# Optimization experiments

Measured on AMD Instinct MI355X. Metric: run time of the kernel, lower is better.

## Reference

```python
import jax, jax.numpy as jnp
import numpy as np

HEADS = 7
DIM_HEAD = 64
SCALE = DIM_HEAD ** -0.5


def setup_inputs() -> dict:
    key = jax.random.key(0)
    ks = jax.random.split(key, 6)
    b, n, dim = 8, 1024, 448
    inner = HEADS * DIM_HEAD  # 448
    x = jax.random.normal(ks[0], (b, n, dim), dtype=jnp.float32)
    w_qv = jax.random.normal(ks[1], (dim, 2 * inner), dtype=jnp.float32) * 0.02
    ext_k = jax.random.normal(ks[2], (HEADS, n, DIM_HEAD), dtype=jnp.float32)
    ext_bias = jax.random.normal(ks[3], (HEADS, n, n), dtype=jnp.float32)
    w_out = jax.random.normal(ks[4], (inner, dim), dtype=jnp.float32) * 0.02
    b_out = jnp.zeros((dim,), dtype=jnp.float32)
    return {"x": x, "w_qv": w_qv, "ext_k": ext_k, "ext_bias": ext_bias,
            "w_out": w_out, "b_out": b_out}


def reference(x, w_qv, ext_k, ext_bias, w_out, b_out):
    b, n, dim = x.shape
    qv = x @ w_qv                                   # [b, n, 2*inner]
    q, v = jnp.split(qv, 2, axis=-1)
    # b n (h d) -> b h n d
    q = q.reshape(b, n, HEADS, DIM_HEAD).transpose(0, 2, 1, 3)
    v = v.reshape(b, n, HEADS, DIM_HEAD).transpose(0, 2, 1, 3)
    # scores vs external learned key, additive bias applied BEFORE scale
    dots = (jnp.einsum('bhnd,hmd->bhnm', q, ext_k) + ext_bias[None]) * SCALE
    attn = jax.nn.softmax(dots, axis=-1)
    out = jnp.einsum('bhnm,bhmd->bhnd', attn, v)
    out = out.transpose(0, 2, 1, 3).reshape(b, n, HEADS * DIM_HEAD)
    return out @ w_out + b_out  # dropout is identity in eval mode
```

## Files before the change

kernel.cpp:

```cpp
#include <hip/hip_runtime.h>
#include <hip/hip_bf16.h>
#include <hip/hip_fp16.h>

#define BATCH 8
#define NSEQ 1024
#define DIMM 448
#define NHEAD 7
#define HDIM 64
#define MROWS (BATCH*NSEQ)
#define KDIM 448
#define SCALE_F 0.125f
#define PSTR 66048

typedef short short8 __attribute__((ext_vector_type(8)));
typedef float floatx16 __attribute__((ext_vector_type(16)));

#define MFMA32(a,b,c) __builtin_amdgcn_mfma_f32_32x32x16_bf16(a,b,c,0,0,0)

__device__ __forceinline__ unsigned short f2bf(float f){
    __hip_bfloat16 h = __float2bfloat16(f);
    return *reinterpret_cast<unsigned short*>(&h);
}
__device__ __forceinline__ float bf2f(unsigned short u){
    __hip_bfloat16 h; *reinterpret_cast<unsigned short*>(&h) = u;
    return __bfloat162float(h);
}
__device__ __forceinline__ float h2f(unsigned short u){
    __half h; *reinterpret_cast<unsigned short*>(&h) = u;
    return __half2float(h);
}
__device__ __forceinline__ unsigned short f2h(float f){
    __half h = __float2half(f);
    return *reinterpret_cast<unsigned short*>(&h);
}

__global__ __launch_bounds__(256)
void prep_all(const float* __restrict__ x, const float* __restrict__ ek,
              const float* __restrict__ wqv, const float* __restrict__ wout,
              const float* __restrict__ eb,
              unsigned short* __restrict__ xh, unsigned short* __restrict__ ekh,
              unsigned short* __restrict__ wqvTh, unsigned short* __restrict__ woTh,
              unsigned short* __restrict__ woTl, unsigned short* __restrict__ bp)
{
    __shared__ float T[2][64][33];
    const int bx = blockIdx.x, tid = threadIdx.x;

    if (bx < 3584) {
        int i = bx*256 + tid;
        float4 v = ((const float4*)x)[i];
        ((ushort4*)xh)[i] = make_ushort4(f2bf(v.x), f2bf(v.y), f2bf(v.z), f2bf(v.w));
    } else if (bx < 4032) {
        int i = (bx-3584)*256 + tid;
        const int h  = i >> 14, mm = (i >> 9) & 31, c = (i >> 7) & 3;
        const int ln = (i >> 1) & 63, jh = i & 1;
        const float* src = ek + ((size_t)(h*NSEQ) + mm*32 + (ln & 31))*HDIM
                              + c*16 + (ln >> 5)*8 + jh*4;
        float4 v = *(const float4*)src;
        unsigned short* dst = ekh + (size_t)h*PSTR + (size_t)(i & 16383)*4;
        *(ushort4*)dst = make_ushort4(f2bf(v.x), f2bf(v.y), f2bf(v.z), f2bf(v.w));
    } else if (bx < 4228) {
        int lid = (bx-4032)*4 + (tid>>6);
        int kc = lid % 56, ng = lid / 56;
        int n = ng*64 + (tid&63);
        unsigned short h[8];
#pragma unroll
        for (int j = 0; j < 8; ++j) h[j] = f2bf(wqv[(size_t)(kc*8+j)*896 + n]);
        size_t o = (size_t)n*KDIM + kc*8;
        *(ushort4*)(wqvTh + o)     = make_ushort4(h[0],h[1],h[2],h[3]);
        *(ushort4*)(wqvTh + o + 4) = make_ushort4(h[4],h[5],h[6],h[7]);
    } else if (bx < 4340) {
        int lid = (bx-4228)*4 + (tid>>6);
        int kc = lid % 56, ng = lid / 56;
        int n = ng*64 + (tid&63);
        ushort4 h0={0,0,0,0}, h1={0,0,0,0}, l0={0,0,0,0}, l1={0,0,0,0};
        if (n < DIMM) {
            unsigned short h[8], l[8];
#pragma unroll
            for (int j = 0; j < 8; ++j) {
                float f = wout[(size_t)(kc*8+j)*DIMM + n];
                h[j] = f2bf(f); l[j] = f2bf(f - bf2f(h[j]));
            }
            h0 = make_ushort4(h[0],h[1],h[2],h[3]); h1 = make_ushort4(h[4],h[5],h[6],h[7]);
            l0 = make_ushort4(l[0],l[1],l[2],l[3]); l1 = make_ushort4(l[4],l[5],l[6],l[7]);
        }
        size_t o = (size_t)n*KDIM + kc*8;
        *(ushort4*)(woTh + o) = h0; *(ushort4*)(woTh + o + 4) = h1;
        *(ushort4*)(woTl + o) = l0; *(ushort4*)(woTl + o + 4) = l1;
    } else {
        const int sub = tid >> 7, st = tid & 127;
        const int lid = (bx-4340)*2 + sub;
        const int mt = lid & 31, qt = (lid>>5) & 15, h = lid >> 9;
#pragma unroll
        for (int it = 0; it < 4; ++it) {
            int idx = it*128 + st;
            int row = idx >> 3, c4 = (idx & 7)*4;
            float4 v = *(const float4*)(eb + ((size_t)(h*NSEQ + qt*64 + row))*NSEQ + mt*32 + c4);
            T[sub][row][c4+0]=v.x; T[sub][row][c4+1]=v.y;
            T[sub][row][c4+2]=v.z; T[sub][row][c4+3]=v.w;
        }
        __syncthreads();
        const int g2 = st >> 6, lane = st & 63;
        const int lq = lane & 31, quad = lane >> 5;
        const int q = g2*32 + lq;
        unsigned short* dst = bp + (size_t)(h*16 + qt)*PSTR
                            + (size_t)(mt*4 + g2*2)*512 + lane*8;
#pragma unroll
        for (int jj = 0; jj < 2; ++jj) {
            unsigned short o[8];
#pragma unroll
            for (int t = 0; t < 8; ++t) {
                int m = (t&3) + 8*(t>>2) + 16*jj + 4*quad;
                o[t] = f2h(T[sub][q][m] * SCALE_F);
            }
            *(ushort4*)(dst + jj*512)     = make_ushort4(o[0],o[1],o[2],o[3]);
            *(ushort4*)(dst + jj*512 + 4) = make_ushort4(o[4],o[5],o[6],o[7]);
        }
    }
}

__global__ __launch_bounds__(256, 2)
void gemm1_grp(const unsigned short* __restrict__ Ah, const unsigned short* __restrict__ Bh,
               unsigned short* __restrict__ qd, unsigned short* __restrict__ vTd)
{
    const int tid = threadIdx.x;
    const int w = tid >> 6, lane = tid & 63;
    const int lq = lane & 31, lh = lane >> 5;
    const int m0 = (blockIdx.x*4 + w) * 64;
    const int y  = blockIdx.y;
    const int n0 = y * 64;
    const unsigned short* aB = Ah + (size_t)(m0 + lq)*KDIM + lh*8;
    const unsigned short* bB = Bh + (size_t)(n0 + lq)*KDIM + lh*8;

    floatx16 acc[2][2] = {};
    short8 aR[2][2][2], bR[2][2][2];
#define LD1(kt, par) {                                                        \
    _Pragma("unroll") for (int fm = 0; fm < 2; ++fm)                          \
    _Pragma("unroll") for (int c = 0; c < 2; ++c) {                           \
        aR[par][fm][c] = *(const short8*)(aB + (size_t)fm*32*KDIM + (kt)*32 + c*16); \
        bR[par][fm][c] = *(const short8*)(bB + (size_t)fm*32*KDIM + (kt)*32 + c*16); } }

    LD1(0, 0)
#pragma unroll
    for (int kt = 0; kt < 14; ++kt) {
        const int par = kt & 1;
        if (kt < 13) LD1(kt+1, par^1)
#pragma unroll
        for (int c = 0; c < 2; ++c)
#pragma unroll
            for (int fm = 0; fm < 2; ++fm)
#pragma unroll
                for (int fn = 0; fn < 2; ++fn)
                    acc[fm][fn] = MFMA32(aR[par][fm][c], bR[par][fn][c], acc[fm][fn]);
    }
#undef LD1

    if (y < NHEAD) {
#pragma unroll
        for (int fm = 0; fm < 2; ++fm)
#pragma unroll
            for (int fn = 0; fn < 2; ++fn) {
                const int d = fn*32 + lq;
#pragma unroll
                for (int r = 0; r < 16; ++r) {
                    const int gm = m0 + fm*32 + (r&3) + 8*(r>>2) + 4*lh;
                    const int b = gm >> 10, ns = gm & 1023;
                    qd[((size_t)((b*NHEAD + y)*NSEQ + ns))*HDIM + d] = f2bf(acc[fm][fn][r]);
                }
            }
    } else {
        const int head = y - NHEAD;
#pragma unroll
        for (int fm = 0; fm < 2; ++fm) {
            const int gm0 = m0 + fm*32;
            const int b = gm0 >> 10, mm = (gm0 & 1023) >> 5;
            unsigned short* base = vTd + (size_t)(b*NHEAD + head)*PSTR + (size_t)mm*2048;
#pragma unroll
            for (int fn = 0; fn < 2; ++fn)
#pragma unroll
                for (int rq = 0; rq < 4; ++rq) {
                    const int u = (rq>>1)*2 + fn;
                    const int lanep = (rq&1)*32 + lq;
                    *(ushort4*)(base + u*512 + lanep*8 + 4*lh) = make_ushort4(
                        f2bf(acc[fm][fn][rq*4+0]), f2bf(acc[fm][fn][rq*4+1]),
                        f2bf(acc[fm][fn][rq*4+2]), f2bf(acc[fm][fn][rq*4+3]));
                }
        }
    }
}

__global__ __launch_bounds__(256, 2)
void attn7q(const unsigned short* __restrict__ qh_g, const unsigned short* __restrict__ vTh,
            const unsigned short* __restrict__ ekh, const unsigned short* __restrict__ bp,
            unsigned short* __restrict__ aoh, unsigned short* __restrict__ aol)
{
    __shared__ unsigned short pS[4][1024];
    __shared__ float linv[4][2][32];

    const int tid = threadIdx.x;
    const int w = tid >> 6, lane = tid & 63;
    const int lq = lane & 31, lh = lane >> 5;

    const int orig = blockIdx.x;
    const int wg = (orig & 7)*28 + (orig >> 3);
    const int bq = wg & 1, qt = (wg >> 1) & 15, head = wg >> 5;
    const int b = bq*4 + w;
    const int bh = b*NHEAD + head;

    short8 qf[2][4];
#pragma unroll
    for (int g2 = 0; g2 < 2; ++g2)
#pragma unroll
        for (int c = 0; c < 4; ++c)
            qf[g2][c] = *(const short8*)(qh_g +
                ((size_t)(bh*NSEQ) + qt*64 + g2*32 + lq)*HDIM + c*16 + lh*8);

    const unsigned short* kB = ekh + (size_t)head*PSTR + lane*8;
    const unsigned short* vB = vTh + (size_t)bh*PSTR + lane*8;
    const unsigned short* bB = bp + (size_t)(head*16 + qt)*PSTR + lane*8;

    short8 kR[2][4], vR[2][4], bR[2][4];
#define PREF(J, par) { const int mm = ((J) < 32) ? (J) : 0;                    \
    _Pragma("unroll") for (int c = 0; c < 4; ++c)                              \
        kR[par][c] = *(const short8*)(kB + (size_t)mm*2048 + c*512);           \
    _Pragma("unroll") for (int u = 0; u < 4; ++u)                              \
        vR[par][u] = *(const short8*)(vB + (size_t)mm*2048 + u*512);           \
    _Pragma("unroll") for (int u = 0; u < 4; ++u)                              \
        bR[par][u] = *(const short8*)(bB + (size_t)mm*2048 + u*512); }

    floatx16 O[2][2] = {};
    float ls[2] = {0.f, 0.f};

#define SEC(J, par, nxt) {                                                     \
    PREF((J)+1, nxt)                                                           \
    _Pragma("unroll") for (int g2 = 0; g2 < 2; ++g2) {                         \
        floatx16 S = {};                                                       \
        _Pragma("unroll") for (int c = 0; c < 4; ++c)                          \
            S = MFMA32(kR[par][c], qf[g2][c], S);                              \
        _Pragma("unroll") for (int g = 0; g < 4; ++g) {                        \
            unsigned short hb[4];                                              \
            _Pragma("unroll") for (int j2 = 0; j2 < 4; ++j2) {                 \
                const int i = g*4 + j2;                                        \
                float bs = h2f((unsigned short)bR[par][g2*2 + (i>>3)][i&7]);   \
                float pv = __expf(fmaf(S[i], SCALE_F, bs));                    \
                ls[g2] += pv;  hb[j2] = f2bf(pv);                              \
            }                                                                  \
            *(ushort4*)(pS[w] + g*256 + lq*8 + lh*4) = make_ushort4(hb[0],hb[1],hb[2],hb[3]); \
        }                                                                      \
        _Pragma("unroll") for (int c2 = 0; c2 < 2; ++c2) {                     \
            short8 pf = *(const short8*)(pS[w] + ((c2*2+lh)*32 + lq)*8);       \
            O[g2][0] = MFMA32(pf, vR[par][c2*2+0], O[g2][0]);                  \
            O[g2][1] = MFMA32(pf, vR[par][c2*2+1], O[g2][1]);                  \
        } } }

    PREF(0, 0)
    for (int jj = 0; jj < 16; ++jj) {
        SEC(2*jj,   0, 1)
        SEC(2*jj+1, 1, 0)
    }
#undef SEC
#undef PREF

    float lt0 = ls[0] + __shfl_xor(ls[0], 32);
    float lt1 = ls[1] + __shfl_xor(ls[1], 32);
    if (lh == 0) { linv[w][0][lq] = 1.f/lt0; linv[w][1][lq] = 1.f/lt1; }

#pragma unroll
    for (int g2 = 0; g2 < 2; ++g2)
#pragma unroll
        for (int r = 0; r < 16; ++r) {
            const int qr = (r&3) + 8*(r>>2) + 4*lh;
            const float inv = linv[w][g2][qr];
            const size_t o = ((size_t)(b*NSEQ) + qt*64 + g2*32 + qr)*DIMM + head*HDIM + lq;
            float v0 = O[g2][0][r]*inv, v1 = O[g2][1][r]*inv;
            unsigned short h0 = f2bf(v0), h1 = f2bf(v1);
            aoh[o]      = h0;  aol[o]      = f2bf(v0 - bf2f(h0));
            aoh[o + 32] = h1;  aol[o + 32] = f2bf(v1 - bf2f(h1));
        }
}

__global__ __launch_bounds__(128, 2)
void gemm2_grp(const unsigned short* __restrict__ Ah, const unsigned short* __restrict__ Al,
               const unsigned short* __restrict__ Bh, const unsigned short* __restrict__ Bl,
               const float* __restrict__ bias, float* __restrict__ out)
{
    const int tid = threadIdx.x;
    const int w = tid >> 6, lane = tid & 63;
    const int lq = lane & 31, lh = lane >> 5;
    const int m0 = (blockIdx.x*2 + w) * 64;
    const int n0 = blockIdx.y * 64;
    const unsigned short* aBh = Ah + (size_t)(m0 + lq)*KDIM + lh*8;
    const unsigned short* aBl = Al + (size_t)(m0 + lq)*KDIM + lh*8;
    const unsigned short* bBh = Bh + (size_t)(n0 + lq)*KDIM + lh*8;
    const unsigned short* bBl = Bl + (size_t)(n0 + lq)*KDIM + lh*8;

    floatx16 acc[2][2] = {};
    short8 aH[2][2][2], aL[2][2][2], bH[2][2][2], bL[2][2][2];
#define LD2(kt, par) {                                                        \
    _Pragma("unroll") for (int fm = 0; fm < 2; ++fm)                          \
    _Pragma("unroll") for (int c = 0; c < 2; ++c) {                           \
        const size_t off = (size_t)fm*32*KDIM + (kt)*32 + c*16;               \
        aH[par][fm][c] = *(const short8*)(aBh + off);                         \
        aL[par][fm][c] = *(const short8*)(aBl + off);                         \
        bH[par][fm][c] = *(const short8*)(bBh + off);                         \
        bL[par][fm][c] = *(const short8*)(bBl + off); } }

    LD2(0, 0)
#pragma unroll
    for (int kt = 0; kt < 14; ++kt) {
        const int par = kt & 1;
        if (kt < 13) LD2(kt+1, par^1)
#pragma unroll
        for (int c = 0; c < 2; ++c)
#pragma unroll
            for (int fm = 0; fm < 2; ++fm)
#pragma unroll
                for (int fn = 0; fn < 2; ++fn) {
                    acc[fm][fn] = MFMA32(aH[par][fm][c], bH[par][fn][c], acc[fm][fn]);
                    acc[fm][fn] = MFMA32(aL[par][fm][c], bH[par][fn][c], acc[fm][fn]);
                    acc[fm][fn] = MFMA32(aH[par][fm][c], bL[par][fn][c], acc[fm][fn]);
                }
    }
#undef LD2

#pragma unroll
    for (int fm = 0; fm < 2; ++fm)
#pragma unroll
        for (int fn = 0; fn < 2; ++fn) {
            const int gn = n0 + fn*32 + lq;
            const float bv = bias[gn];
#pragma unroll
            for (int r = 0; r < 16; ++r) {
                const int gm = m0 + fm*32 + (r&3) + 8*(r>>2) + 4*lh;
                out[(size_t)gm*DIMM + gn] = acc[fm][fn][r] + bv;
            }
        }
}

extern "C" void kernel_launch(void* const* d_in, const int* in_sizes, int n_in,
                              void* d_out, int out_size, void* d_ws, size_t ws_size,
                              hipStream_t stream)
{
    const float* x    = (const float*)d_in[0];
    const float* wqv  = (const float*)d_in[1];
    const float* ek   = (const float*)d_in[2];
    const float* eb   = (const float*)d_in[3];
    const float* wout = (const float*)d_in[4];
    const float* bout = (const float*)d_in[5];
    float* out = (float*)d_out;

    const size_t MK = (size_t)MROWS*KDIM;
    unsigned short* p = (unsigned short*)d_ws;
    unsigned short* xh    = p;  p += MK;
    unsigned short* wqvTh = p;  p += (size_t)896*KDIM;
    unsigned short* woTh  = p;  p += (size_t)512*KDIM;
    unsigned short* woTl  = p;  p += (size_t)512*KDIM;
    unsigned short* ekh   = p;  p += (size_t)NHEAD*PSTR;
    unsigned short* qh    = p;  p += MK;
    unsigned short* vTh   = p;  p += (size_t)BATCH*NHEAD*PSTR;
    unsigned short* bp    = p;  p += (size_t)NHEAD*16*PSTR;
    unsigned short* aoh   = p;  p += MK;
    unsigned short* aol   = p;  p += MK;

    prep_all<<<6132, 256, 0, stream>>>(x, ek, wqv, wout, eb,
                                       xh, ekh, wqvTh, woTh, woTl, bp);
    gemm1_grp<<<dim3(32, 14), 256, 0, stream>>>(xh, wqvTh, qh, vTh);
    attn7q<<<224, 256, 0, stream>>>(qh, vTh, ekh, bp, aoh, aol);
    gemm2_grp<<<dim3(64, 7), 128, 0, stream>>>(aoh, aol, woTh, woTl, bout, out);
}
```

Measured before the change: 189.4 us.

## Move bias, ext_k and w_out prep into the QV GEMM launch to overlap

Trims the prep kernel so it only converts x and w_qv, which the first GEMM depends on. The independent preprocessing work (bias transpose and scaling to fp16, ext_k packing, w_out hi/lo split) now runs as extra blocks in the same launch as the QV GEMM. The GEMM blocks come first and the conversion blocks follow, so memory-bound conversion can fill the GPU alongside the MFMA-bound GEMM blocks. The GEMM blocks use a flattened 1D grid index, and the 64x33 float shared-memory buffer is now declared in the GEMM kernel as well, which may reduce occupancy for the GEMM blocks.

```diff
diff --git a/kernel.cpp b/kernel.cpp
--- a/kernel.cpp
+++ b/kernel.cpp
@@ -35,22 +35,133 @@
 }
 
 __global__ __launch_bounds__(256)
-void prep_all(const float* __restrict__ x, const float* __restrict__ ek,
-              const float* __restrict__ wqv, const float* __restrict__ wout,
-              const float* __restrict__ eb,
-              unsigned short* __restrict__ xh, unsigned short* __restrict__ ekh,
-              unsigned short* __restrict__ wqvTh, unsigned short* __restrict__ woTh,
-              unsigned short* __restrict__ woTl, unsigned short* __restrict__ bp)
-{
-    __shared__ float T[2][64][33];
+void prep_min(const float* __restrict__ x, const float* __restrict__ wqv,
+              unsigned short* __restrict__ xh, unsigned short* __restrict__ wqvTh)
+{
     const int bx = blockIdx.x, tid = threadIdx.x;
-
     if (bx < 3584) {
         int i = bx*256 + tid;
         float4 v = ((const float4*)x)[i];
         ((ushort4*)xh)[i] = make_ushort4(f2bf(v.x), f2bf(v.y), f2bf(v.z), f2bf(v.w));
-    } else if (bx < 4032) {
-        int i = (bx-3584)*256 + tid;
+    } else {
+        int lid = (bx-3584)*4 + (tid>>6);
+        int kc = lid % 56, ng = lid / 56;
+        int n = ng*64 + (tid&63);
+        unsigned short h[8];
+#pragma unroll
+        for (int j = 0; j < 8; ++j) h[j] = f2bf(wqv[(size_t)(kc*8+j)*896 + n]);
+        size_t o = (size_t)n*KDIM + kc*8;
+        *(ushort4*)(wqvTh + o)     = make_ushort4(h[0],h[1],h[2],h[3]);
+        *(ushort4*)(wqvTh + o + 4) = make_ushort4(h[4],h[5],h[6],h[7]);
+    }
+}
+
+__global__ __launch_bounds__(256, 2)
+void gemm1_fused(const unsigned short* __restrict__ Ah, const unsigned short* __restrict__ Bh,
+                 const float* __restrict__ ek, const float* __restrict__ eb,
+                 const float* __restrict__ wout,
+                 unsigned short* __restrict__ qd, unsigned short* __restrict__ vTd,
+                 unsigned short* __restrict__ ekh, unsigned short* __restrict__ bp,
+                 unsigned short* __restrict__ woTh, unsigned short* __restrict__ woTl)
+{
+    __shared__ float T[2][64][33];
+    const int bx = blockIdx.x, tid = threadIdx.x;
+
+    if (bx < 448) {
+        const int w = tid >> 6, lane = tid & 63;
+        const int lq = lane & 31, lh = lane >> 5;
+        const int xb = bx & 31, y = bx >> 5;
+        const int m0 = (xb*4 + w) * 64;
+        const int n0 = y * 64;
+        const unsigned short* aB = Ah + (size_t)(m0 + lq)*KDIM + lh*8;
+        const unsigned short* bB = Bh + (size_t)(n0 + lq)*KDIM + lh*8;
+
+        floatx16 acc[2][2] = {};
+        short8 aR[2][2][2], bR[2][2][2];
+#define LD1(kt, par) {                                                        \
+    _Pragma("unroll") for (int fm = 0; fm < 2; ++fm)                          \
+    _Pragma("unroll") for (int c = 0; c < 2; ++c) {                           \
+        aR[par][fm][c] = *(const short8*)(aB + (size_t)fm*32*KDIM + (kt)*32 + c*16); \
+        bR[par][fm][c] = *(const short8*)(bB + (size_t)fm*32*KDIM + (kt)*32 + c*16); } }
+
+        LD1(0, 0)
+#pragma unroll
+        for (int kt = 0; kt < 14; ++kt) {
+            const int par = kt & 1;
+            if (kt < 13) LD1(kt+1, par^1)
+#pragma unroll
+            for (int c = 0; c < 2; ++c)
+#pragma unroll
+                for (int fm = 0; fm < 2; ++fm)
+#pragma unroll
+                    for (int fn = 0; fn < 2; ++fn)
+                        acc[fm][fn] = MFMA32(aR[par][fm][c], bR[par][fn][c], acc[fm][fn]);
+        }
+#undef LD1
+
+        if (y < NHEAD) {
+#pragma unroll
+            for (int fm = 0; fm < 2; ++fm)
+#pragma unroll
+                for (int fn = 0; fn < 2; ++fn) {
+                    const int d = fn*32 + lq;
+#pragma unroll
+                    for (int r = 0; r < 16; ++r) {
+                        const int gm = m0 + fm*32 + (r&3) + 8*(r>>2) + 4*lh;
+                        const int b = gm >> 10, ns = gm & 1023;
+                        qd[((size_t)((b*NHEAD + y)*NSEQ + ns))*HDIM + d] = f2bf(acc[fm][fn][r]);
+                    }
+                }
+        } else {
+            const int head = y - NHEAD;
+#pragma unroll
+            for (int fm = 0; fm < 2; ++fm) {
+                const int gm0 = m0 + fm*32;
+                const int b = gm0 >> 10, mm = (gm0 & 1023) >> 5;
+                unsigned short* base = vTd + (size_t)(b*NHEAD + head)*PSTR + (size_t)mm*2048;
+#pragma unroll
+                for (int fn = 0; fn < 2; ++fn)
+#pragma unroll
+                    for (int rq = 0; rq < 4; ++rq) {
+                        const int u = (rq>>1)*2 + fn;
+                        const int lanep = (rq&1)*32 + lq;
+                        *(ushort4*)(base + u*512 + lanep*8 + 4*lh) = make_ushort4(
+                            f2bf(acc[fm][fn][rq*4+0]), f2bf(acc[fm][fn][rq*4+1]),
+                            f2bf(acc[fm][fn][rq*4+2]), f2bf(acc[fm][fn][rq*4+3]));
+                    }
+            }
+        }
+    } else if (bx < 2240) {
+        const int sub = tid >> 7, st = tid & 127;
+        const int lid = (bx-448)*2 + sub;
+        const int mt = lid & 31, qt = (lid>>5) & 15, h = lid >> 9;
+#pragma unroll
+        for (int it = 0; it < 4; ++it) {
+            int idx = it*128 + st;
+            int row = idx >> 3, c4 = (idx & 7)*4;
+            float4 v = *(const float4*)(eb + ((size_t)(h*NSEQ + qt*64 + row))*NSEQ + mt*32 + c4);
+            T[sub][row][c4+0]=v.x; T[sub][row][c4+1]=v.y;
+            T[sub][row][c4+2]=v.z; T[sub][row][c4+3]=v.w;
+        }
+        __syncthreads();
+        const int g2 = st >> 6, lane = st & 63;
+        const int lq = lane & 31, quad = lane >> 5;
+        const int q = g2*32 + lq;
+        unsigned short* dst = bp + (size_t)(h*16 + qt)*PSTR
+                            + (size_t)(mt*4 + g2*2)*512 + lane*8;
+#pragma unroll
+        for (int jj = 0; jj < 2; ++jj) {
+            unsigned short o[8];
+#pragma unroll
+            for (int t = 0; t < 8; ++t) {
+                int m = (t&3) + 8*(t>>2) + 16*jj + 4*quad;
+                o[t] = f2h(T[sub][q][m] * SCALE_F);
+            }
+            *(ushort4*)(dst + jj*512)     = make_ushort4(o[0],o[1],o[2],o[3]);
+            *(ushort4*)(dst + jj*512 + 4) = make_ushort4(o[4],o[5],o[6],o[7]);
+        }
+    } else if (bx < 2688) {
+        int i = (bx-2240)*256 + tid;
         const int h  = i >> 14, mm = (i >> 9) & 31, c = (i >> 7) & 3;
         const int ln = (i >> 1) & 63, jh = i & 1;
         const float* src = ek + ((size_t)(h*NSEQ) + mm*32 + (ln & 31))*HDIM
@@ -58,18 +169,8 @@
         float4 v = *(const float4*)src;
         unsigned short* dst = ekh + (size_t)h*PSTR + (size_t)(i & 16383)*4;
         *(ushort4*)dst = make_ushort4(f2bf(v.x), f2bf(v.y), f2bf(v.z), f2bf(v.w));
-    } else if (bx < 4228) {
-        int lid = (bx-4032)*4 + (tid>>6);
-        int kc = lid % 56, ng = lid / 56;
-        int n = ng*64 + (tid&63);
-        unsigned short h[8];
-#pragma unroll
-        for (int j = 0; j < 8; ++j) h[j] = f2bf(wqv[(size_t)(kc*8+j)*896 + n]);
-        size_t o = (size_t)n*KDIM + kc*8;
-        *(ushort4*)(wqvTh + o)     = make_ushort4(h[0],h[1],h[2],h[3]);
-        *(ushort4*)(wqvTh + o + 4) = make_ushort4(h[4],h[5],h[6],h[7]);
-    } else if (bx < 4340) {
-        int lid = (bx-4228)*4 + (tid>>6);
+    } else {
+        int lid = (bx-2688)*4 + (tid>>6);
         int kc = lid % 56, ng = lid / 56;
         int n = ng*64 + (tid&63);
         ushort4 h0={0,0,0,0}, h1={0,0,0,0}, l0={0,0,0,0}, l1={0,0,0,0};
@@ -86,105 +187,6 @@
         size_t o = (size_t)n*KDIM + kc*8;
         *(ushort4*)(woTh + o) = h0; *(ushort4*)(woTh + o + 4) = h1;
         *(ushort4*)(woTl + o) = l0; *(ushort4*)(woTl + o + 4) = l1;
-    } else {
-        const int sub = tid >> 7, st = tid & 127;
-        const int lid = (bx-4340)*2 + sub;
-        const int mt = lid & 31, qt = (lid>>5) & 15, h = lid >> 9;
-#pragma unroll
-        for (int it = 0; it < 4; ++it) {
-            int idx = it*128 + st;
-            int row = idx >> 3, c4 = (idx & 7)*4;
-            float4 v = *(const float4*)(eb + ((size_t)(h*NSEQ + qt*64 + row))*NSEQ + mt*32 + c4);
-            T[sub][row][c4+0]=v.x; T[sub][row][c4+1]=v.y;
-            T[sub][row][c4+2]=v.z; T[sub][row][c4+3]=v.w;
-        }
-        __syncthreads();
-        const int g2 = st >> 6, lane = st & 63;
-        const int lq = lane & 31, quad = lane >> 5;
-        const int q = g2*32 + lq;
-        unsigned short* dst = bp + (size_t)(h*16 + qt)*PSTR
-                            + (size_t)(mt*4 + g2*2)*512 + lane*8;
-#pragma unroll
-        for (int jj = 0; jj < 2; ++jj) {
-            unsigned short o[8];
-#pragma unroll
-            for (int t = 0; t < 8; ++t) {
-                int m = (t&3) + 8*(t>>2) + 16*jj + 4*quad;
-                o[t] = f2h(T[sub][q][m] * SCALE_F);
-            }
-            *(ushort4*)(dst + jj*512)     = make_ushort4(o[0],o[1],o[2],o[3]);
-            *(ushort4*)(dst + jj*512 + 4) = make_ushort4(o[4],o[5],o[6],o[7]);
-        }
-    }
-}
-
-__global__ __launch_bounds__(256, 2)
-void gemm1_grp(const unsigned short* __restrict__ Ah, const unsigned short* __restrict__ Bh,
-               unsigned short* __restrict__ qd, unsigned short* __restrict__ vTd)
-{
-    const int tid = threadIdx.x;
-    const int w = tid >> 6, lane = tid & 63;
-    const int lq = lane & 31, lh = lane >> 5;
-    const int m0 = (blockIdx.x*4 + w) * 64;
-    const int y  = blockIdx.y;
-    const int n0 = y * 64;
-    const unsigned short* aB = Ah + (size_t)(m0 + lq)*KDIM + lh*8;
-    const unsigned short* bB = Bh + (size_t)(n0 + lq)*KDIM + lh*8;
-
-    floatx16 acc[2][2] = {};
-    short8 aR[2][2][2], bR[2][2][2];
-#define LD1(kt, par) {                                                        \
-    _Pragma("unroll") for (int fm = 0; fm < 2; ++fm)                          \
-    _Pragma("unroll") for (int c = 0; c < 2; ++c) {                           \
-        aR[par][fm][c] = *(const short8*)(aB + (size_t)fm*32*KDIM + (kt)*32 + c*16); \
-        bR[par][fm][c] = *(const short8*)(bB + (size_t)fm*32*KDIM + (kt)*32 + c*16); } }
-
-    LD1(0, 0)
-#pragma unroll
-    for (int kt = 0; kt < 14; ++kt) {
-        const int par = kt & 1;
-        if (kt < 13) LD1(kt+1, par^1)
-#pragma unroll
-        for (int c = 0; c < 2; ++c)
-#pragma unroll
-            for (int fm = 0; fm < 2; ++fm)
-#pragma unroll
-                for (int fn = 0; fn < 2; ++fn)
-                    acc[fm][fn] = MFMA32(aR[par][fm][c], bR[par][fn][c], acc[fm][fn]);
-    }
-#undef LD1
-
-    if (y < NHEAD) {
-#pragma unroll
-        for (int fm = 0; fm < 2; ++fm)
-#pragma unroll
-            for (int fn = 0; fn < 2; ++fn) {
-                const int d = fn*32 + lq;
-#pragma unroll
-                for (int r = 0; r < 16; ++r) {
-                    const int gm = m0 + fm*32 + (r&3) + 8*(r>>2) + 4*lh;
-                    const int b = gm >> 10, ns = gm & 1023;
-                    qd[((size_t)((b*NHEAD + y)*NSEQ + ns))*HDIM + d] = f2bf(acc[fm][fn][r]);
-                }
-            }
-    } else {
-        const int head = y - NHEAD;
-#pragma unroll
-        for (int fm = 0; fm < 2; ++fm) {
-            const int gm0 = m0 + fm*32;
-            const int b = gm0 >> 10, mm = (gm0 & 1023) >> 5;
-            unsigned short* base = vTd + (size_t)(b*NHEAD + head)*PSTR + (size_t)mm*2048;
-#pragma unroll
-            for (int fn = 0; fn < 2; ++fn)
-#pragma unroll
-                for (int rq = 0; rq < 4; ++rq) {
-                    const int u = (rq>>1)*2 + fn;
-                    const int lanep = (rq&1)*32 + lq;
-                    *(ushort4*)(base + u*512 + lanep*8 + 4*lh) = make_ushort4(
-                        f2bf(acc[fm][fn][rq*4+0]), f2bf(acc[fm][fn][rq*4+1]),
-                        f2bf(acc[fm][fn][rq*4+2]), f2bf(acc[fm][fn][rq*4+3]));
-                }
-        }
     }
 }
 
@@ -361,9 +363,9 @@
     unsigned short* aoh   = p;  p += MK;
     unsigned short* aol   = p;  p += MK;
 
-    prep_all<<<6132, 256, 0, stream>>>(x, ek, wqv, wout, eb,
-                                       xh, ekh, wqvTh, woTh, woTl, bp);
-    gemm1_grp<<<dim3(32, 14), 256, 0, stream>>>(xh, wqvTh, qh, vTh);
+    prep_min<<<3780, 256, 0, stream>>>(x, wqv, xh, wqvTh);
+    gemm1_fused<<<2800, 256, 0, stream>>>(xh, wqvTh, ek, eb, wout,
+                                          qh, vTh, ekh, bp, woTh, woTl);
     attn7q<<<224, 256, 0, stream>>>(qh, vTh, ekh, bp, aoh, aol);
     gemm2_grp<<<dim3(64, 7), 128, 0, stream>>>(aoh, aol, woTh, woTl, bout, out);
 }
```

Result: no change. 186.3 us (-1.7%).
